# Optimization experiments

Measured on AMD Instinct MI355X. Metric: run time of the kernel, lower is better.

Reference implementation:

```python
import jax, jax.numpy as jnp
import numpy as np

N = 8192
D_IN = 1024
D_OUT = 1024


def setup_inputs() -> dict:
    key = jax.random.key(0)
    ks = jax.random.split(key, 7)
    s = 1.0 / np.sqrt(D_IN)
    return {
        "feat": jax.random.normal(ks[0], (N, D_IN), dtype=jnp.float32),
        "Wq": jax.random.uniform(ks[1], (D_IN, D_OUT), jnp.float32, -s, s),
        "bq": jax.random.uniform(ks[2], (D_OUT,), jnp.float32, -s, s),
        "Wk": jax.random.uniform(ks[3], (D_IN, D_OUT), jnp.float32, -s, s),
        "bk": jax.random.uniform(ks[4], (D_OUT,), jnp.float32, -s, s),
        "Wv": jax.random.uniform(ks[5], (D_IN, D_OUT), jnp.float32, -s, s),
        "bv": jax.random.uniform(ks[6], (D_OUT,), jnp.float32, -s, s),
    }


def reference(feat, Wq, bq, Wk, bk, Wv, bv):
    # eval mode: dropout(p=0.3, training=False) is identity
    q = feat @ Wq + bq          # [N, D_OUT]
    k = feat @ Wk + bk          # [N, D_OUT]
    v = feat @ Wv + bv          # [N, D_OUT]
    scale = 1.0 / jnp.sqrt(jnp.float32(D_OUT))
    scores = (q @ k.T) * scale  # [N, N]
    attn = jax.nn.softmax(scores, axis=1)
    return attn @ v             # [N, D_OUT]
```

## Files before the change

kernel.cpp:

```cpp
#include <hip/hip_runtime.h>
#include <hip/hip_bf16.h>
#include <stdint.h>

typedef __hip_bfloat16 bf16;
typedef __attribute__((ext_vector_type(8))) short short8;
typedef __attribute__((ext_vector_type(4))) float f32x4;

#define BM 128
#define BN 128

__device__ __forceinline__ unsigned short f2bf_bits(float x) {
    return __builtin_bit_cast(unsigned short, __float2bfloat16(x));
}

__device__ __forceinline__ void gload_lds16(const bf16* g, bf16* l) {
    __builtin_amdgcn_global_load_lds(
        (const __attribute__((address_space(1))) void*)(const void*)g,
        (__attribute__((address_space(3))) void*)(void*)l,
        16, 0, 0);
}

__global__ void prep_kernel(const float* __restrict__ feat, unsigned short* __restrict__ featb,
                            const float* __restrict__ W0, const float* __restrict__ W1,
                            const float* __restrict__ W2, bf16* __restrict__ Wt,
                            float* __restrict__ lsum) {
    const int b = blockIdx.x;
    const int tid = threadIdx.x;
    if (b < 8192) {
        int i = b * 256 + tid;
        float4 v = reinterpret_cast<const float4*>(feat)[i];
        ushort4 o;
        o.x = f2bf_bits(v.x); o.y = f2bf_bits(v.y);
        o.z = f2bf_bits(v.z); o.w = f2bf_bits(v.w);
        reinterpret_cast<ushort4*>(featb)[i] = o;
    } else if (b < 11264) {
        __shared__ float tile[32][33];
        const int b2 = b - 8192;
        const int z = b2 >> 10;
        const int t = b2 & 1023;
        const int bx = t & 31, by = t >> 5;
        const int tx = tid & 31, ty = tid >> 5;
        const float* in = (z == 0) ? W0 : (z == 1) ? W1 : W2;
        bf16* out = Wt + (size_t)z * 1024 * 1024;
        for (int r = ty; r < 32; r += 8)
            tile[r][tx] = in[(size_t)(by * 32 + r) * 1024 + bx * 32 + tx];
        __syncthreads();
        for (int r = ty; r < 32; r += 8)
            out[(size_t)(bx * 32 + r) * 1024 + by * 32 + tx] = __float2bfloat16(tile[tx][r]);
    } else {
        for (int i = tid; i < 8192; i += 256) lsum[i] = 0.f;
    }
}

__global__ void tpose_bf16(const bf16* __restrict__ in, bf16* __restrict__ out, int rows, int cols) {
    __shared__ bf16 tile[32][33];
    const int bx = blockIdx.x, by = blockIdx.y, tx = threadIdx.x;
    for (int r = threadIdx.y; r < 32; r += 8)
        tile[r][tx] = in[(size_t)(by * 32 + r) * cols + bx * 32 + tx];
    __syncthreads();
    for (int r = threadIdx.y; r < 32; r += 8)
        out[(size_t)(bx * 32 + r) * rows + by * 32 + tx] = tile[tx][r];
}

__global__ void scale_rows(float* __restrict__ out, const float* __restrict__ lsum) {
    int i = blockIdx.x * 256 + threadIdx.x;
    float4 v = reinterpret_cast<float4*>(out)[i];
    float inv = 1.0f / lsum[i >> 8];
    v.x *= inv; v.y *= inv; v.z *= inv; v.w *= inv;
    reinterpret_cast<float4*>(out)[i] = v;
}

template <int MODE, int KH, int SWAP>
__global__ __launch_bounds__(256, 4)
void gemm_bt(const bf16* __restrict__ A, const bf16* __restrict__ B,
             const float* __restrict__ b0, const float* __restrict__ b1,
             const float* __restrict__ b2, float* __restrict__ lsum,
             bf16* __restrict__ outb, float* __restrict__ outf,
             int M, int N, int K, int ldb, int ldout, float scale) {
    constexpr int TILE = 128 * 32;
    constexpr int SELEMS = (2 * KH * TILE < 9216) ? 9216 : 2 * KH * TILE;
    __shared__ bf16 smem[SELEMS];
    bf16* As = smem;
    bf16* Bs = smem + KH * TILE;

    const int tid  = threadIdx.x;
    const int lane = tid & 63;
    const int wave = tid >> 6;
    const int wm = wave & 1, wn = wave >> 1;
    const int l16  = lane & 15;
    const int quad = lane >> 4;
    long bm0, bn0;
    if (SWAP == 2) {
        const int lin = blockIdx.y * 8 + blockIdx.x;
        const int xcd = lin & 7;
        const int s   = lin >> 3;
        bn0 = (long)(s & 7) * BN;
        bm0 = (long)((s >> 3) * 8 + xcd) * BM;
    } else {
        bm0 = (long)(SWAP ? blockIdx.y : blockIdx.x) * BM;
        bn0 = (long)(SWAP ? blockIdx.x : blockIdx.y) * BN;
    }

    const float* bias = nullptr;
    if (MODE == 0) {
        const int z = blockIdx.z;
        B    += (size_t)z * N * K;
        outb += (size_t)z * M * ldout;
        bias  = (z == 0) ? b0 : (z == 1) ? b1 : b2;
    }

    const int  ksp   = (MODE == 4) ? (K >> 1) : K;
    const long k0beg = (MODE == 4) ? (long)blockIdx.z * ksp : 0;

    const int lrow = lane >> 2;
    const int lcol = (lane & 3) * 8;
    const bf16* gA[2][KH];
    const bf16* gB[2][KH];
    bf16* lA[2][KH];
    bf16* lB[2][KH];
#pragma unroll
    for (int u = 0; u < 2; u++)
#pragma unroll
        for (int h = 0; h < KH; h++) {
            gA[u][h] = A + (size_t)(bm0 + wave * 32 + u * 16 + lrow) * K + h * 32 + lcol;
            gB[u][h] = B + (size_t)(bn0 + wave * 32 + u * 16 + lrow) * ldb + h * 32 + lcol;
            lA[u][h] = As + h * TILE + (wave * 32 + u * 16) * 32;
            lB[u][h] = Bs + h * TILE + (wave * 32 + u * 16) * 32;
        }

    const bf16* Ard = As + (wm * 64 + l16) * 32 + quad * 8;
    const bf16* Brd = Bs + (wn * 64 + l16) * 32 + quad * 8;

    f32x4 acc[4][4];
    const f32x4 zero = {0.f, 0.f, 0.f, 0.f};
#pragma unroll
    for (int i = 0; i < 4; i++)
#pragma unroll
        for (int j = 0; j < 4; j++) acc[i][j] = zero;

    for (long k0 = k0beg; k0 < k0beg + ksp; k0 += KH * 32) {
        __syncthreads();
#pragma unroll
        for (int u = 0; u < 2; u++)
#pragma unroll
            for (int h = 0; h < KH; h++) {
                gload_lds16(gA[u][h] + k0, lA[u][h]);
                gload_lds16(gB[u][h] + k0, lB[u][h]);
            }
        __syncthreads();
#pragma unroll
        for (int h = 0; h < KH; h++) {
            short8 af[4], bfr[4];
#pragma unroll
            for (int mi = 0; mi < 4; mi++)
                af[mi] = *reinterpret_cast<const short8*>(Ard + h * TILE + mi * 16 * 32);
#pragma unroll
            for (int ni = 0; ni < 4; ni++)
                bfr[ni] = *reinterpret_cast<const short8*>(Brd + h * TILE + ni * 16 * 32);
#pragma unroll
            for (int mi = 0; mi < 4; mi++)
#pragma unroll
                for (int ni = 0; ni < 4; ni++)
                    acc[mi][ni] = __builtin_amdgcn_mfma_f32_16x16x32_bf16(af[mi], bfr[ni], acc[mi][ni], 0, 0, 0);
        }
    }

    if (MODE == 0 || MODE == 1) {
        __syncthreads();
        bf16* eb = smem + wave * 1152;
        float bcol[4];
        if (MODE == 0) {
#pragma unroll
            for (int ni = 0; ni < 4; ni++) bcol[ni] = bias[bn0 + wn * 64 + l16 + ni * 16];
        }
#pragma unroll
        for (int mi = 0; mi < 4; mi++) {
#pragma unroll
            for (int r = 0; r < 4; r++) {
                float s = 0.f;
#pragma unroll
                for (int ni = 0; ni < 4; ni++) {
                    float v = acc[mi][ni][r];
                    if (MODE == 0) v += bcol[ni];
                    else { v = __expf(v * scale); s += v; }
                    eb[(quad * 4 + r) * 72 + ni * 16 + l16] = __float2bfloat16(v);
                }
                if (MODE == 1) {
                    s += __shfl_xor(s, 1);
                    s += __shfl_xor(s, 2);
                    s += __shfl_xor(s, 4);
                    s += __shfl_xor(s, 8);
                    if (l16 == 0) atomicAdd(&lsum[bm0 + wm * 64 + mi * 16 + quad * 4 + r], s);
                }
            }
            asm volatile("s_waitcnt lgkmcnt(0)" ::: "memory");
#pragma unroll
            for (int p = 0; p < 2; p++) {
                int r2 = p * 8 + (lane >> 3);
                int c2 = (lane & 7) * 8;
                short8 val = *reinterpret_cast<const short8*>(eb + r2 * 72 + c2);
                *reinterpret_cast<short8*>(
                    outb + (size_t)(bm0 + wm * 64 + mi * 16 + r2) * ldout + bn0 + wn * 64 + c2) = val;
            }
            asm volatile("s_waitcnt lgkmcnt(0)" ::: "memory");
        }
    } else {
        const int rb2 = wm * 64 + quad * 4;
        const int cb2 = wn * 64 + l16;
#pragma unroll
        for (int mi = 0; mi < 4; mi++)
#pragma unroll
            for (int r = 0; r < 4; r++) {
                long row = bm0 + rb2 + mi * 16 + r;
                float mul = (MODE == 3) ? 1.0f / lsum[row] : 0.f;
#pragma unroll
                for (int ni = 0; ni < 4; ni++) {
                    long col = bn0 + cb2 + ni * 16;
                    if (MODE == 3)      outf[row * ldout + col] = acc[mi][ni][r] * mul;
                    else if (MODE == 4) atomicAdd(&outf[row * ldout + col], acc[mi][ni][r]);
                    else                outf[row * ldout + col] += acc[mi][ni][r];
                }
            }
    }
}

extern "C" void kernel_launch(void* const* d_in, const int* in_sizes, int n_in,
                              void* d_out, int out_size, void* d_ws, size_t ws_size,
                              hipStream_t stream) {
    const float* feat = (const float*)d_in[0];
    const float* Wq   = (const float*)d_in[1];
    const float* bqv  = (const float*)d_in[2];
    const float* Wk   = (const float*)d_in[3];
    const float* bkv  = (const float*)d_in[4];
    const float* Wv   = (const float*)d_in[5];
    const float* bvv  = (const float*)d_in[6];
    float* outp = (float*)d_out;

    const int M = 8192, D = 1024;
    char* ws = (char*)d_ws;
    size_t off = 0;
    auto carve = [&](size_t bytes) -> char* {
        char* r = ws + off;
        off += (bytes + 255) & ~(size_t)255;
        return r;
    };
    bf16* featb = (bf16*)carve((size_t)M * D * 2);
    bf16* Wbt   = (bf16*)carve((size_t)3 * D * D * 2);
    bf16* qkv   = (bf16*)carve((size_t)3 * M * D * 2);
    float* lsum = (float*)carve((size_t)M * 4);
    bf16* vbt   = featb;
    size_t avail = (ws_size > off) ? ws_size - off : 0;

    int C;
    if      (avail >= (size_t)M * M * 2)    C = M;
    else if (avail >= (size_t)M * 4096 * 2) C = 4096;
    else if (avail >= (size_t)M * 2048 * 2) C = 2048;
    else                                    C = 1024;
    bf16* Pc = (bf16*)carve((size_t)M * C * 2);

    prep_kernel<<<dim3(11265), dim3(256), 0, stream>>>(
        feat, (unsigned short*)featb, Wq, Wk, Wv, Wbt, lsum);
    gemm_bt<0, 2, 0><<<dim3(M / 128, D / 128, 3), dim3(256), 0, stream>>>(
        featb, Wbt, bqv, bkv, bvv, nullptr, qkv, nullptr, M, D, D, D, D, 1.0f);
    tpose_bf16<<<dim3(D / 32, M / 32), dim3(32, 8), 0, stream>>>(qkv + (size_t)2 * M * D, vbt, M, D);

    const float scale = 0.03125f;
    bf16* qb = qkv;
    bf16* kb = qkv + (size_t)M * D;
    if (C == M) {
        gemm_bt<1, 2, 0><<<dim3(M / 128, M / 128), dim3(256), 0, stream>>>(
            qb, kb, nullptr, nullptr, nullptr, lsum, Pc, nullptr, M, M, D, D, M, scale);
        hipMemsetAsync(outp, 0, (size_t)M * D * 4, stream);
        gemm_bt<4, 2, 2><<<dim3(D / 128, M / 128, 2), dim3(256), 0, stream>>>(
            Pc, vbt, nullptr, nullptr, nullptr, nullptr, nullptr, outp, M, D, M, M, D, 0.f);
        scale_rows<<<dim3(M * D / 4 / 256), dim3(256), 0, stream>>>(outp, lsum);
    } else {
        hipMemsetAsync(outp, 0, (size_t)M * D * 4, stream);
        for (int c = 0; c < M / C; c++) {
            gemm_bt<1, 2, 0><<<dim3(M / 128, C / 128), dim3(256), 0, stream>>>(
                qb, kb + (size_t)c * C * D, nullptr, nullptr, nullptr, lsum, Pc, nullptr,
                M, C, D, D, C, scale);
            gemm_bt<2, 2, 1><<<dim3(D / 128, M / 128), dim3(256), 0, stream>>>(
                Pc, vbt + (size_t)c * C, nullptr, nullptr, nullptr, nullptr, nullptr, outp,
                M, D, C, M, D, 0.f);
        }
        scale_rows<<<dim3(M * D / 4 / 256), dim3(256), 0, stream>>>(outp, lsum);
    }
}
```

Before: 476.1 us.

## Compute V transposed directly in GEMM and fuse row normalization into PV GEMM

The V projection is now computed as Wv^T·feat^T in a new GEMM mode that adds a per-row bias and writes V already transposed, so the separate transpose kernel goes away. In the full-materialization path, the split-K PV GEMM with atomic adds, the output memset and the scale_rows pass are replaced by one non-split GEMM that multiplies by 1/lsum in its epilogue. This cuts launches, atomic traffic and a full read/write pass over the output. The cost is half as many blocks for the PV GEMM (64 per N-tile row instead of 128), so it loses some parallelism, and V now needs its own workspace buffer.

```diff
diff --git a/kernel.cpp b/kernel.cpp
--- a/kernel.cpp
+++ b/kernel.cpp
@@ -52,16 +52,6 @@
     }
 }
 
-__global__ void tpose_bf16(const bf16* __restrict__ in, bf16* __restrict__ out, int rows, int cols) {
-    __shared__ bf16 tile[32][33];
-    const int bx = blockIdx.x, by = blockIdx.y, tx = threadIdx.x;
-    for (int r = threadIdx.y; r < 32; r += 8)
-        tile[r][tx] = in[(size_t)(by * 32 + r) * cols + bx * 32 + tx];
-    __syncthreads();
-    for (int r = threadIdx.y; r < 32; r += 8)
-        out[(size_t)(bx * 32 + r) * rows + by * 32 + tx] = tile[tx][r];
-}
-
 __global__ void scale_rows(float* __restrict__ out, const float* __restrict__ lsum) {
     int i = blockIdx.x * 256 + threadIdx.x;
     float4 v = reinterpret_cast<float4*>(out)[i];
@@ -106,11 +96,8 @@
         const int z = blockIdx.z;
         B    += (size_t)z * N * K;
         outb += (size_t)z * M * ldout;
-        bias  = (z == 0) ? b0 : (z == 1) ? b1 : b2;
-    }
-
-    const int  ksp   = (MODE == 4) ? (K >> 1) : K;
-    const long k0beg = (MODE == 4) ? (long)blockIdx.z * ksp : 0;
+        bias  = (z == 0) ? b0 : b1;
+    }
 
     const int lrow = lane >> 2;
     const int lcol = (lane & 3) * 8;
@@ -138,7 +125,7 @@
 #pragma unroll
         for (int j = 0; j < 4; j++) acc[i][j] = zero;
 
-    for (long k0 = k0beg; k0 < k0beg + ksp; k0 += KH * 32) {
+    for (int k0 = 0; k0 < K; k0 += KH * 32) {
         __syncthreads();
 #pragma unroll
         for (int u = 0; u < 2; u++)
@@ -165,7 +152,7 @@
         }
     }
 
-    if (MODE == 0 || MODE == 1) {
+    if (MODE == 0 || MODE == 1 || MODE == 5) {
         __syncthreads();
         bf16* eb = smem + wave * 1152;
         float bcol[4];
@@ -178,10 +165,13 @@
 #pragma unroll
             for (int r = 0; r < 4; r++) {
                 float s = 0.f;
+                float brow = 0.f;
+                if (MODE == 5) brow = b2[bm0 + wm * 64 + mi * 16 + quad * 4 + r];
 #pragma unroll
                 for (int ni = 0; ni < 4; ni++) {
                     float v = acc[mi][ni][r];
-                    if (MODE == 0) v += bcol[ni];
+                    if (MODE == 0)      v += bcol[ni];
+                    else if (MODE == 5) v += brow;
                     else { v = __expf(v * scale); s += v; }
                     eb[(quad * 4 + r) * 72 + ni * 16 + l16] = __float2bfloat16(v);
                 }
@@ -216,9 +206,8 @@
 #pragma unroll
                 for (int ni = 0; ni < 4; ni++) {
                     long col = bn0 + cb2 + ni * 16;
-                    if (MODE == 3)      outf[row * ldout + col] = acc[mi][ni][r] * mul;
-                    else if (MODE == 4) atomicAdd(&outf[row * ldout + col], acc[mi][ni][r]);
-                    else                outf[row * ldout + col] += acc[mi][ni][r];
+                    if (MODE == 3) outf[row * ldout + col] = acc[mi][ni][r] * mul;
+                    else           outf[row * ldout + col] += acc[mi][ni][r];
                 }
             }
     }
@@ -246,9 +235,9 @@
     };
     bf16* featb = (bf16*)carve((size_t)M * D * 2);
     bf16* Wbt   = (bf16*)carve((size_t)3 * D * D * 2);
-    bf16* qkv   = (bf16*)carve((size_t)3 * M * D * 2);
+    bf16* qk    = (bf16*)carve((size_t)2 * M * D * 2);
+    bf16* vbt   = (bf16*)carve((size_t)D * M * 2);
     float* lsum = (float*)carve((size_t)M * 4);
-    bf16* vbt   = featb;
     size_t avail = (ws_size > off) ? ws_size - off : 0;
 
     int C;
@@ -260,20 +249,20 @@
 
     prep_kernel<<<dim3(11265), dim3(256), 0, stream>>>(
         feat, (unsigned short*)featb, Wq, Wk, Wv, Wbt, lsum);
-    gemm_bt<0, 2, 0><<<dim3(M / 128, D / 128, 3), dim3(256), 0, stream>>>(
-        featb, Wbt, bqv, bkv, bvv, nullptr, qkv, nullptr, M, D, D, D, D, 1.0f);
-    tpose_bf16<<<dim3(D / 32, M / 32), dim3(32, 8), 0, stream>>>(qkv + (size_t)2 * M * D, vbt, M, D);
+    gemm_bt<0, 2, 0><<<dim3(M / 128, D / 128, 2), dim3(256), 0, stream>>>(
+        featb, Wbt, bqv, bkv, nullptr, nullptr, qk, nullptr, M, D, D, D, D, 1.0f);
+    gemm_bt<5, 2, 0><<<dim3(D / 128, M / 128), dim3(256), 0, stream>>>(
+        Wbt + (size_t)2 * D * D, featb, nullptr, nullptr, bvv, nullptr, vbt, nullptr,
+        D, M, D, D, M, 1.0f);
 
     const float scale = 0.03125f;
-    bf16* qb = qkv;
-    bf16* kb = qkv + (size_t)M * D;
+    bf16* qb = qk;
+    bf16* kb = qk + (size_t)M * D;
     if (C == M) {
         gemm_bt<1, 2, 0><<<dim3(M / 128, M / 128), dim3(256), 0, stream>>>(
             qb, kb, nullptr, nullptr, nullptr, lsum, Pc, nullptr, M, M, D, D, M, scale);
-        hipMemsetAsync(outp, 0, (size_t)M * D * 4, stream);
-        gemm_bt<4, 2, 2><<<dim3(D / 128, M / 128, 2), dim3(256), 0, stream>>>(
-            Pc, vbt, nullptr, nullptr, nullptr, nullptr, nullptr, outp, M, D, M, M, D, 0.f);
-        scale_rows<<<dim3(M * D / 4 / 256), dim3(256), 0, stream>>>(outp, lsum);
+        gemm_bt<3, 2, 2><<<dim3(D / 128, M / 128), dim3(256), 0, stream>>>(
+            Pc, vbt, nullptr, nullptr, nullptr, lsum, nullptr, outp, M, D, M, M, D, 0.f);
     } else {
         hipMemsetAsync(outp, 0, (size_t)M * D * 4, stream);
         for (int c = 0; c < M / C; c++) {
```

Result: faster. 445.9 us (-6.3%).
